# Performance work log

Hardware: AMD Instinct MI355X
Metric: run time of the kernel (lower is better)

## Reference

```python
import jax, jax.numpy as jnp
import numpy as np

NUM_CLASSES = 10
NPTS = 100            # quadrature points per unit interval (torch default npts=100)
EPS = 1e-5            # self.epsilon in the torch module
BATCH = 131072
C_IN = 512


def _betaln(a, b):
    return jax.lax.lgamma(a) + jax.lax.lgamma(b) - jax.lax.lgamma(a + b)


def setup_inputs() -> dict:
    key = jax.random.key(0)
    k1, k2, k3, k4, k5 = jax.random.split(key, 5)
    s = 1.0 / np.sqrt(C_IN).astype(np.float32)
    x = jax.random.normal(k1, (BATCH, C_IN), dtype=jnp.float32)
    W_alpha = jax.random.normal(k2, (C_IN, 1), dtype=jnp.float32) * s
    b_alpha = jax.random.normal(k3, (1,), dtype=jnp.float32) * s
    W_beta = jax.random.normal(k4, (C_IN, 1), dtype=jnp.float32) * s
    b_beta = jax.random.normal(k5, (1,), dtype=jnp.float32) * s
    return {"x": x, "W_alpha": W_alpha, "b_alpha": b_alpha,
            "W_beta": W_beta, "b_beta": b_beta}


def reference(x, W_alpha, b_alpha, W_beta, b_beta):
    # alpha, beta: [B, 1], clamp(1 + softplus(linear(x)), 1, 100)
    alpha = jnp.clip(1.0 + jax.nn.softplus(x @ W_alpha + b_alpha), 1.0, 100.0)
    beta = jnp.clip(1.0 + jax.nn.softplus(x @ W_beta + b_beta), 1.0, 100.0)
    lbeta = _betaln(alpha, beta)  # [B, 1] log Beta-function normalizer
    dx = 1.0 / (NPTS * NUM_CLASSES)

    def unnorm_cdf(b_thr):
        # torch: linspace(eps, b-eps, int(npts*b)); Beta.log_prob broadcast [B, n]
        n = int(NPTS * b_thr)
        if n == 0:
            return jnp.zeros((x.shape[0],), dtype=x.dtype)
        grid = jnp.linspace(EPS, b_thr - EPS, n, dtype=x.dtype)  # [n]
        logpdf = ((alpha - 1.0) * jnp.log(grid)
                  + (beta - 1.0) * jnp.log1p(-grid)
                  - lbeta)  # [B, n]
        return jnp.exp(logpdf).sum(axis=1) * dx  # [B]

    # thresholds i/C for i = 0..C (static Python loop over C+1 small fixed set)
    cdfs = [unnorm_cdf(i / NUM_CLASSES) for i in range(NUM_CLASSES + 1)]
    probs = jnp.stack([cdfs[i + 1] - cdfs[i] for i in range(NUM_CLASSES)], axis=1)  # [B, C]
    # torch uses diag(1/rowsum) @ probs == row-broadcast normalization
    return probs / probs.sum(axis=1, keepdims=True)
```

## Files before the change

### kernel.cpp

```cpp
#include <hip/hip_runtime.h>
#include <math.h>

#define EPS_F 1e-5f
#define NPOINTS 550
#define CIN 512

static __device__ __forceinline__ float softplus_f(float z) {
    return fmaxf(z, 0.0f) + log1pf(expf(-fabsf(z)));
}

static __device__ __forceinline__ float dot8(const float4 a0, const float4 a1,
                                             const float4 w0, const float4 w1) {
    float s = a0.x * w0.x;
    s = fmaf(a0.y, w0.y, s);
    s = fmaf(a0.z, w0.z, s);
    s = fmaf(a0.w, w0.w, s);
    s = fmaf(a1.x, w1.x, s);
    s = fmaf(a1.y, w1.y, s);
    s = fmaf(a1.z, w1.z, s);
    s = fmaf(a1.w, w1.w, s);
    return s;
}

__global__ __launch_bounds__(256, 4) void gemv_kernel(
    const float* __restrict__ x,
    const float* __restrict__ Wa,
    const float* __restrict__ Wb,
    float* __restrict__ ws)
{
    __shared__ float part[4][4][68];

    const int tid = threadIdx.x;
    const int lane = tid & 63;
    const int wave = tid >> 6;
    const long waveRow0 = (long)blockIdx.x * 128 + wave * 32;

    const float4* Wa4 = (const float4*)Wa;
    const float4* Wb4 = (const float4*)Wb;
    const float4 wa0 = Wa4[lane], wa1 = Wa4[64 + lane];
    const float4 wb0 = Wb4[lane], wb1 = Wb4[64 + lane];

    const int g = lane >> 4;
    const int k = lane & 15;

    float4 buf[2][4];
    {
        const float4* xr = (const float4*)(x + waveRow0 * CIN);
        buf[0][0] = xr[lane];
        buf[0][1] = xr[64 + lane];
        buf[0][2] = xr[128 + lane];
        buf[0][3] = xr[192 + lane];
    }

    #pragma unroll
    for (int t = 0; t < 16; ++t) {
        const int cur = t & 1;
        if (t + 1 < 16) {
            const float4* xn = (const float4*)(x + (waveRow0 + (t + 1) * 2) * CIN);
            buf[cur ^ 1][0] = xn[lane];
            buf[cur ^ 1][1] = xn[64 + lane];
            buf[cur ^ 1][2] = xn[128 + lane];
            buf[cur ^ 1][3] = xn[192 + lane];
        }

        const float pa0 = dot8(buf[cur][0], buf[cur][1], wa0, wa1);
        const float pb0 = dot8(buf[cur][0], buf[cur][1], wb0, wb1);
        const float pa1 = dot8(buf[cur][2], buf[cur][3], wa0, wa1);
        const float pb1 = dot8(buf[cur][2], buf[cur][3], wb0, wb1);

        part[wave][0][lane] = pa0;
        part[wave][1][lane] = pb0;
        part[wave][2][lane] = pa1;
        part[wave][3][lane] = pb1;
        asm volatile("s_waitcnt lgkmcnt(0)" ::: "memory");

        const float4 q = *(const float4*)&part[wave][g][k * 4];
        float s = (q.x + q.y) + (q.z + q.w);
        s += __shfl_xor(s, 8, 64);
        s += __shfl_xor(s, 4, 64);
        s += __shfl_xor(s, 2, 64);
        s += __shfl_xor(s, 1, 64);

        if (k == 0) ws[(waveRow0 + t * 2) * 2 + g] = s;
    }
}

__global__ __launch_bounds__(256, 4) void quad_kernel(
    const float* __restrict__ ws,
    const float* __restrict__ ba, const float* __restrict__ bb,
    float* __restrict__ out)
{
    __shared__ __align__(16) float2 tab[NPOINTS];
    __shared__ float outb[256 * 10];

    const int tid = threadIdx.x;

    for (int p = tid; p < NPOINTS; p += 256) {
        int i = 1, off = 0;
        while (p >= off + 10 * i) { off += 10 * i; ++i; }
        const int j = p - off;
        const int n = 10 * i;
        const float thr = (float)i * 0.1f;
        const float step = (thr - 2.0f * EPS_F) / (float)(n - 1);
        const float gx = EPS_F + step * (float)j;
        float2 e;
        e.x = log2f(gx);
        e.y = log2f(1.0f - gx);
        tab[p] = e;
    }
    __syncthreads();

    const long row = (long)blockIdx.x * 256 + tid;
    const float2 d = ((const float2*)ws)[row];
    const float za = d.x + ba[0];
    const float zb = d.y + bb[0];
    const float alpha = fminf(fmaxf(1.0f + softplus_f(za), 1.0f), 100.0f);
    const float beta  = fminf(fmaxf(1.0f + softplus_f(zb), 1.0f), 100.0f);
    const float am1 = alpha - 1.0f;
    const float bm1 = beta - 1.0f;

    const float denom = am1 + bm1;
    float mode = (denom > 0.0f) ? (am1 / denom) : 0.5f;
    mode = fminf(fmaxf(mode, 1e-7f), 1.0f - 1.1920929e-7f);
    const float nM2 = -(am1 * log2f(mode) + bm1 * log2f(1.0f - mode));

    float seg[10];
    int p0 = 0;
    #pragma unroll
    for (int i = 1; i <= 10; ++i) {
        const int n = 10 * i;
        float s2 = 0.0f;
        for (int j = 0; j < n; j += 2) {
            const float4 tq = *(const float4*)&tab[p0 + j];
            const float e0 = fmaf(am1, tq.x, fmaf(bm1, tq.y, nM2));
            const float e1 = fmaf(am1, tq.z, fmaf(bm1, tq.w, nM2));
            s2 += __builtin_amdgcn_exp2f(e0) + __builtin_amdgcn_exp2f(e1);
        }
        seg[i - 1] = s2;
        p0 += n;
    }

    const float inv = 1.0f / seg[9];
    float prev = 0.0f;
    #pragma unroll
    for (int kk = 0; kk < 10; ++kk) {
        outb[tid * 10 + kk] = (seg[kk] - prev) * inv;
        prev = seg[kk];
    }
    __syncthreads();

    const float4* s4 = (const float4*)outb;
    float4* dst = (float4*)(out + (size_t)blockIdx.x * 2560);
    #pragma unroll
    for (int idx = tid; idx < 640; idx += 256) dst[idx] = s4[idx];
}

extern "C" void kernel_launch(void* const* d_in, const int* in_sizes, int n_in,
                              void* d_out, int out_size, void* d_ws, size_t ws_size,
                              hipStream_t stream) {
    const float* x  = (const float*)d_in[0];
    const float* Wa = (const float*)d_in[1];
    const float* ba = (const float*)d_in[2];
    const float* Wb = (const float*)d_in[3];
    const float* bb = (const float*)d_in[4];
    float* out = (float*)d_out;
    float* ws  = (float*)d_ws;

    const int batch = in_sizes[0] / CIN;
    gemv_kernel<<<batch / 128, 256, 0, stream>>>(x, Wa, Wb, ws);
    quad_kernel<<<batch / 256, 256, 0, stream>>>(ws, ba, bb, out);
}
```

Before: 421.5 us.

## Defer GEMV cross-lane reduction to quad kernel via 16-way partial sums

The GEMV kernel now gives each row to 16 lanes. Each lane writes its own (alpha, beta) partial dot product to the workspace, so the per-row LDS round-trip and shuffle reduction are gone. The kernel uses a grid-stride loop with 2048 blocks, keeps the weights in LDS, and raises the occupancy hint. The quad kernel then sums the 16 partials per row itself. This trades extra workspace traffic (128 bytes per row) for a simpler, more bandwidth-bound GEMV.

```diff
diff --git a/kernel.cpp b/kernel.cpp
--- a/kernel.cpp
+++ b/kernel.cpp
@@ -9,84 +9,55 @@
     return fmaxf(z, 0.0f) + log1pf(expf(-fabsf(z)));
 }
 
-static __device__ __forceinline__ float dot8(const float4 a0, const float4 a1,
-                                             const float4 w0, const float4 w1) {
-    float s = a0.x * w0.x;
-    s = fmaf(a0.y, w0.y, s);
-    s = fmaf(a0.z, w0.z, s);
-    s = fmaf(a0.w, w0.w, s);
-    s = fmaf(a1.x, w1.x, s);
-    s = fmaf(a1.y, w1.y, s);
-    s = fmaf(a1.z, w1.z, s);
-    s = fmaf(a1.w, w1.w, s);
-    return s;
-}
+__global__ __launch_bounds__(256, 8) void gemv_part_kernel(
+    const float* __restrict__ x,
+    const float* __restrict__ Wa, const float* __restrict__ Wb,
+    float2* __restrict__ part,
+    int nRowGrp)
+{
+    __shared__ float4 WaL[128], WbL[128];
+    const int tid = threadIdx.x;
+    if (tid < 128) {
+        WaL[tid] = ((const float4*)Wa)[tid];
+        WbL[tid] = ((const float4*)Wb)[tid];
+    }
+    __syncthreads();
 
-__global__ __launch_bounds__(256, 4) void gemv_kernel(
-    const float* __restrict__ x,
-    const float* __restrict__ Wa,
-    const float* __restrict__ Wb,
-    float* __restrict__ ws)
-{
-    __shared__ float part[4][4][68];
-
-    const int tid = threadIdx.x;
     const int lane = tid & 63;
     const int wave = tid >> 6;
-    const long waveRow0 = (long)blockIdx.x * 128 + wave * 32;
+    const int r = lane >> 4;
+    const int c = lane & 15;
+    const int stride = gridDim.x * 4;
 
-    const float4* Wa4 = (const float4*)Wa;
-    const float4* Wb4 = (const float4*)Wb;
-    const float4 wa0 = Wa4[lane], wa1 = Wa4[64 + lane];
-    const float4 wb0 = Wb4[lane], wb1 = Wb4[64 + lane];
+    for (int rg = blockIdx.x * 4 + wave; rg < nRowGrp; rg += stride) {
+        const long row = (long)rg * 4 + r;
+        const float4* xp = (const float4*)(x + row * CIN) + c;
 
-    const int g = lane >> 4;
-    const int k = lane & 15;
+        float4 xv[8];
+        #pragma unroll
+        for (int j = 0; j < 8; ++j)
+            xv[j] = xp[16 * j];
 
-    float4 buf[2][4];
-    {
-        const float4* xr = (const float4*)(x + waveRow0 * CIN);
-        buf[0][0] = xr[lane];
-        buf[0][1] = xr[64 + lane];
-        buf[0][2] = xr[128 + lane];
-        buf[0][3] = xr[192 + lane];
-    }
-
-    #pragma unroll
-    for (int t = 0; t < 16; ++t) {
-        const int cur = t & 1;
-        if (t + 1 < 16) {
-            const float4* xn = (const float4*)(x + (waveRow0 + (t + 1) * 2) * CIN);
-            buf[cur ^ 1][0] = xn[lane];
-            buf[cur ^ 1][1] = xn[64 + lane];
-            buf[cur ^ 1][2] = xn[128 + lane];
-            buf[cur ^ 1][3] = xn[192 + lane];
+        float pa = 0.0f, pb = 0.0f;
+        #pragma unroll
+        for (int j = 0; j < 8; ++j) {
+            const float4 wa = WaL[16 * j + c];
+            const float4 wb = WbL[16 * j + c];
+            pa = fmaf(xv[j].x, wa.x, pa);
+            pa = fmaf(xv[j].y, wa.y, pa);
+            pa = fmaf(xv[j].z, wa.z, pa);
+            pa = fmaf(xv[j].w, wa.w, pa);
+            pb = fmaf(xv[j].x, wb.x, pb);
+            pb = fmaf(xv[j].y, wb.y, pb);
+            pb = fmaf(xv[j].z, wb.z, pb);
+            pb = fmaf(xv[j].w, wb.w, pb);
         }
-
-        const float pa0 = dot8(buf[cur][0], buf[cur][1], wa0, wa1);
-        const float pb0 = dot8(buf[cur][0], buf[cur][1], wb0, wb1);
-        const float pa1 = dot8(buf[cur][2], buf[cur][3], wa0, wa1);
-        const float pb1 = dot8(buf[cur][2], buf[cur][3], wb0, wb1);
-
-        part[wave][0][lane] = pa0;
-        part[wave][1][lane] = pb0;
-        part[wave][2][lane] = pa1;
-        part[wave][3][lane] = pb1;
-        asm volatile("s_waitcnt lgkmcnt(0)" ::: "memory");
-
-        const float4 q = *(const float4*)&part[wave][g][k * 4];
-        float s = (q.x + q.y) + (q.z + q.w);
-        s += __shfl_xor(s, 8, 64);
-        s += __shfl_xor(s, 4, 64);
-        s += __shfl_xor(s, 2, 64);
-        s += __shfl_xor(s, 1, 64);
-
-        if (k == 0) ws[(waveRow0 + t * 2) * 2 + g] = s;
+        part[row * 16 + c] = make_float2(pa, pb);
     }
 }
 
 __global__ __launch_bounds__(256, 4) void quad_kernel(
-    const float* __restrict__ ws,
+    const float2* __restrict__ part,
     const float* __restrict__ ba, const float* __restrict__ bb,
     float* __restrict__ out)
 {
@@ -111,9 +82,17 @@
     __syncthreads();
 
     const long row = (long)blockIdx.x * 256 + tid;
-    const float2 d = ((const float2*)ws)[row];
-    const float za = d.x + ba[0];
-    const float zb = d.y + bb[0];
+    const float4* pp = (const float4*)(part + row * 16);
+    float da = 0.0f, db = 0.0f;
+    #pragma unroll
+    for (int j = 0; j < 8; ++j) {
+        const float4 v = pp[j];
+        da += v.x + v.z;
+        db += v.y + v.w;
+    }
+
+    const float za = da + ba[0];
+    const float zb = db + bb[0];
     const float alpha = fminf(fmaxf(1.0f + softplus_f(za), 1.0f), 100.0f);
     const float beta  = fminf(fmaxf(1.0f + softplus_f(zb), 1.0f), 100.0f);
     const float am1 = alpha - 1.0f;
@@ -164,9 +143,10 @@
     const float* Wb = (const float*)d_in[3];
     const float* bb = (const float*)d_in[4];
     float* out = (float*)d_out;
-    float* ws  = (float*)d_ws;
+    float2* part = (float2*)d_ws;
 
     const int batch = in_sizes[0] / CIN;
-    gemv_kernel<<<batch / 128, 256, 0, stream>>>(x, Wa, Wb, ws);
-    quad_kernel<<<batch / 256, 256, 0, stream>>>(ws, ba, bb, out);
+    const int nRowGrp = batch / 4;
+    gemv_part_kernel<<<2048, 256, 0, stream>>>(x, Wa, Wb, part, nRowGrp);
+    quad_kernel<<<batch / 256, 256, 0, stream>>>(part, ba, bb, out);
 }
```

New measurement: 427.5 us. Within noise of the previous version (+1.4%).
